# Kernel tuning notes

Hardware: AMD Instinct MI355X
Metric: run time of the kernel (lower is better)

The kernel has to match this reference:

```python
import jax, jax.numpy as jnp
import numpy as np

NUM_PARTS = 24  # SMPL body parts


def setup_inputs() -> dict:
    key = jax.random.key(0)
    k1, k2, k3 = jax.random.split(key, 3)
    B, N, C = 64, 16384, 128
    xyz = jax.random.normal(k1, (B, N, 3), dtype=jnp.float32)
    features = jax.random.normal(k2, (B, C, N), dtype=jnp.float32)
    labels = jax.random.randint(k3, (B, N), 0, NUM_PARTS, dtype=jnp.int32)
    return {"xyz": xyz, "features": features, "labels": labels}


def reference(xyz, features, labels):
    # xyz: [B,N,3], features: [B,C,N], labels: [B,N] int in [0,24)
    B, N, _ = xyz.shape
    C = features.shape[1]
    K = NUM_PARTS

    onehot = (labels[:, :, None] == jnp.arange(K)[None, None, :]).astype(xyz.dtype)  # [B,N,K]
    counts = onehot.sum(axis=1)                       # [B,K]
    denom = jnp.maximum(counts, 1.0)[:, :, None]      # torch.where(count!=0, count, 1)

    feats_t = jnp.transpose(features, (0, 2, 1))      # [B,N,C]
    mean_xyz = jnp.einsum('bnk,bnc->bkc', onehot, xyz) / denom      # [B,K,3]
    mean_feat = jnp.einsum('bnk,bnc->bkc', onehot, feats_t) / denom  # [B,K,C]
    # (empty segments already yield 0 since the sum is 0; matches non_zero_mask logic)

    # surface branch: per point, subtract its own segment's mean, mask outside
    # segment to 0, then max over all points (zeros included in the original max)
    mean_per_point = jnp.take_along_axis(mean_feat, labels[:, :, None].astype(jnp.int32), axis=1)  # [B,N,C]
    diff = feats_t - mean_per_point                   # [B,N,C]
    seg_ids = (jnp.arange(B, dtype=jnp.int32)[:, None] * K + labels).reshape(-1)  # [B*N]
    seg_max = jax.ops.segment_max(diff.reshape(B * N, C), seg_ids, num_segments=B * K)
    surface = jnp.maximum(seg_max.reshape(B, K, C), 0.0)  # zeros from masked points dominate; empty seg -> 0

    part_features = jnp.concatenate([mean_feat, surface], axis=-1)   # [B,K,2C]
    concat = jnp.concatenate([mean_xyz, part_features], axis=-1)     # [B,K,3+2C] = concatenate_features
    return concat
```

## Files before the change

kernel.cpp:

```cpp
#include <hip/hip_runtime.h>

#define BB 64
#define NN 16384
#define CC 128
#define KK 24
#define OUTW (3 + 2*CC)
#define NCHUNK 16

__global__ __launch_bounds__(256) void k1_cnt_xyz(
    const float* __restrict__ xyz, const int* __restrict__ labels,
    float* __restrict__ pcnt, float* __restrict__ psxyz)
{
    __shared__ float bins[4][KK][4];
    const int tid   = threadIdx.x;
    const int b     = blockIdx.x >> 4;
    const int chunk = blockIdx.x & 15;
    const int w     = tid >> 6;

    for (int i = tid; i < 4*KK*4; i += 256) ((float*)bins)[i] = 0.f;
    __syncthreads();

    const int4*   lrow = (const int4*)(labels + (size_t)b*NN);
    const float4* xrow = (const float4*)(xyz + (size_t)b*NN*3);

    int n4 = chunk*256 + tid;
    int4 l = lrow[n4];
    float4 f0 = xrow[n4*3+0], f1 = xrow[n4*3+1], f2 = xrow[n4*3+2];
    float px[4] = {f0.x, f0.w, f1.z, f2.y};
    float py[4] = {f0.y, f1.x, f1.w, f2.z};
    float pz[4] = {f0.z, f1.y, f2.x, f2.w};
    int   ls[4] = {l.x, l.y, l.z, l.w};
    #pragma unroll
    for (int j = 0; j < 4; ++j) {
        float* bb = bins[w][ls[j]];
        atomicAdd(&bb[0], 1.0f);
        atomicAdd(&bb[1], px[j]);
        atomicAdd(&bb[2], py[j]);
        atomicAdd(&bb[3], pz[j]);
    }
    __syncthreads();
    if (tid < KK*4) {
        int k = tid >> 2, j = tid & 3;
        float v = bins[0][k][j] + bins[1][k][j] + bins[2][k][j] + bins[3][k][j];
        int base = (b*NCHUNK + chunk)*KK + k;
        if (j == 0) pcnt[base] = v;
        else        psxyz[base*3 + (j-1)] = v;
    }
}

__global__ __launch_bounds__(256) void k2_feat(
    const float* __restrict__ features, const int* __restrict__ labels,
    float* __restrict__ sumf, float* __restrict__ maxf)
{
    const int tid  = threadIdx.x;
    const int lane = tid & 63;
    const int wid  = blockIdx.x*4 + (tid >> 6);
    const int b    = wid >> 6;
    const int cp   = wid & 63;

    const float4* f0 = (const float4*)(features + ((size_t)b*CC + cp)*NN);
    const float4* f1 = f0 + (size_t)64*NN/4;
    const int4*   lr = (const int4*)(labels + (size_t)b*NN);

    float s0[KK], s1[KK], m0[KK], m1[KK];
    #pragma unroll
    for (int k = 0; k < KK; ++k) { s0[k]=0.f; s1[k]=0.f; m0[k]=0.f; m1[k]=0.f; }

    for (int it = 0; it < NN/256; ++it) {
        int idx = it*64 + lane;
        float4 a = f0[idx];
        float4 c = f1[idx];
        int4   l = lr[idx];
        #pragma unroll
        for (int k = 0; k < KK; ++k) {
            bool e0 = (l.x == k), e1 = (l.y == k), e2 = (l.z == k), e3 = (l.w == k);
            float t0 = e0 ? a.x : 0.f, t1 = e1 ? a.y : 0.f;
            float t2 = e2 ? a.z : 0.f, t3 = e3 ? a.w : 0.f;
            s0[k] += (t0 + t1) + (t2 + t3);
            m0[k] = fmaxf(fmaxf(m0[k], t0), t1);
            m0[k] = fmaxf(fmaxf(m0[k], t2), t3);
            float u0 = e0 ? c.x : 0.f, u1 = e1 ? c.y : 0.f;
            float u2 = e2 ? c.z : 0.f, u3 = e3 ? c.w : 0.f;
            s1[k] += (u0 + u1) + (u2 + u3);
            m1[k] = fmaxf(fmaxf(m1[k], u0), u1);
            m1[k] = fmaxf(fmaxf(m1[k], u2), u3);
        }
    }

    #pragma unroll
    for (int k = 0; k < KK; ++k) {
        #pragma unroll
        for (int off = 32; off; off >>= 1) {
            s0[k] += __shfl_xor(s0[k], off, 64);
            s1[k] += __shfl_xor(s1[k], off, 64);
            m0[k] = fmaxf(m0[k], __shfl_xor(m0[k], off, 64));
            m1[k] = fmaxf(m1[k], __shfl_xor(m1[k], off, 64));
        }
    }

    if (lane == 0) {
        float* sp = sumf + (size_t)b*KK*CC + cp;
        float* mp = maxf + (size_t)b*KK*CC + cp;
        #pragma unroll
        for (int k = 0; k < KK; ++k) {
            sp[k*CC]      = s0[k];
            sp[k*CC + 64] = s1[k];
            mp[k*CC]      = m0[k];
            mp[k*CC + 64] = m1[k];
        }
    }
}

__global__ __launch_bounds__(128) void k3_final(
    const float* __restrict__ pcnt, const float* __restrict__ psxyz,
    const float* __restrict__ sumf, const float* __restrict__ maxf,
    float* __restrict__ out)
{
    const int bk = blockIdx.x;
    const int b  = bk / KK, k = bk % KK;
    const int c  = threadIdx.x;

    float cn = 0.f;
    #pragma unroll
    for (int ch = 0; ch < NCHUNK; ++ch) cn += pcnt[(b*NCHUNK + ch)*KK + k];
    float inv = 1.0f / fmaxf(cn, 1.0f);

    float* orow = out + (size_t)bk * OUTW;
    if (c < 3) {
        float s = 0.f;
        #pragma unroll
        for (int ch = 0; ch < NCHUNK; ++ch) s += psxyz[((b*NCHUNK + ch)*KK + k)*3 + c];
        orow[c] = s * inv;
    }
    float s    = sumf[(size_t)bk*CC + c];
    float mean = s * inv;
    orow[3 + c] = mean;
    float m    = maxf[(size_t)bk*CC + c];
    orow[3 + CC + c] = (cn > 0.f) ? fmaxf(m - mean, 0.f) : 0.f;
}

extern "C" void kernel_launch(void* const* d_in, const int* in_sizes, int n_in,
                              void* d_out, int out_size, void* d_ws, size_t ws_size,
                              hipStream_t stream) {
    const float* xyz      = (const float*)d_in[0];
    const float* features = (const float*)d_in[1];
    const int*   labels   = (const int*)d_in[2];
    float* out = (float*)d_out;

    char* ws = (char*)d_ws;
    const size_t SZ_SUMF = (size_t)BB*KK*CC*4;
    const size_t SZ_PCNT = (size_t)BB*NCHUNK*KK*4;
    float* sumf  = (float*)ws;
    float* maxf  = (float*)(ws + SZ_SUMF);
    float* pcnt  = (float*)(ws + 2*SZ_SUMF);
    float* psxyz = (float*)(ws + 2*SZ_SUMF + SZ_PCNT);

    k1_cnt_xyz<<<BB*NCHUNK, 256, 0, stream>>>(xyz, labels, pcnt, psxyz);
    k2_feat<<<BB*CC/2/4, 256, 0, stream>>>(features, labels, sumf, maxf);
    k3_final<<<BB*KK, 128, 0, stream>>>(pcnt, psxyz, sumf, maxf, out);
}
```

Measured before the change: 962.2 us.

## Replace per-segment register scan with LDS atomic binning in feature reduction

The feature kernel no longer loops over all 24 segments per element with compare-and-select into register accumulators. Each element is now scattered into shared-memory bins keyed by its label using atomicAdd for sums and integer atomicMax for clamped maxima, with 4 replica slots per wave to spread contention. This removes the 24x redundant ALU work and the large register footprint. In exchange it adds heavy LDS atomic traffic with bank conflicts and serialization when lanes share a label. Float atomic summation order also becomes nondeterministic.

```diff
diff --git a/kernel.cpp b/kernel.cpp
--- a/kernel.cpp
+++ b/kernel.cpp
@@ -52,62 +52,61 @@
     const float* __restrict__ features, const int* __restrict__ labels,
     float* __restrict__ sumf, float* __restrict__ maxf)
 {
+    __shared__ float s_sum[4][KK][4][2];
+    __shared__ int   s_max[4][KK][4][2];
+
     const int tid  = threadIdx.x;
     const int lane = tid & 63;
-    const int wid  = blockIdx.x*4 + (tid >> 6);
+    const int w    = tid >> 6;
+    const int wid  = blockIdx.x*4 + w;
     const int b    = wid >> 6;
     const int cp   = wid & 63;
+    const int r2   = (lane & 3) * 2;
+
+    for (int i = tid; i < 4*KK*4*2; i += 256) {
+        ((float*)s_sum)[i] = 0.f;
+        ((int*)  s_max)[i] = 0;
+    }
+    __syncthreads();
 
     const float4* f0 = (const float4*)(features + ((size_t)b*CC + cp)*NN);
     const float4* f1 = f0 + (size_t)64*NN/4;
     const int4*   lr = (const int4*)(labels + (size_t)b*NN);
 
-    float s0[KK], s1[KK], m0[KK], m1[KK];
-    #pragma unroll
-    for (int k = 0; k < KK; ++k) { s0[k]=0.f; s1[k]=0.f; m0[k]=0.f; m1[k]=0.f; }
+    float* ws_sum = &s_sum[w][0][0][0];
+    int*   ws_max = &s_max[w][0][0][0];
 
     for (int it = 0; it < NN/256; ++it) {
         int idx = it*64 + lane;
         float4 a = f0[idx];
         float4 c = f1[idx];
         int4   l = lr[idx];
+        int   la[4] = {l.x, l.y, l.z, l.w};
+        float va[4] = {a.x, a.y, a.z, a.w};
+        float vc[4] = {c.x, c.y, c.z, c.w};
         #pragma unroll
-        for (int k = 0; k < KK; ++k) {
-            bool e0 = (l.x == k), e1 = (l.y == k), e2 = (l.z == k), e3 = (l.w == k);
-            float t0 = e0 ? a.x : 0.f, t1 = e1 ? a.y : 0.f;
-            float t2 = e2 ? a.z : 0.f, t3 = e3 ? a.w : 0.f;
-            s0[k] += (t0 + t1) + (t2 + t3);
-            m0[k] = fmaxf(fmaxf(m0[k], t0), t1);
-            m0[k] = fmaxf(fmaxf(m0[k], t2), t3);
-            float u0 = e0 ? c.x : 0.f, u1 = e1 ? c.y : 0.f;
-            float u2 = e2 ? c.z : 0.f, u3 = e3 ? c.w : 0.f;
-            s1[k] += (u0 + u1) + (u2 + u3);
-            m1[k] = fmaxf(fmaxf(m1[k], u0), u1);
-            m1[k] = fmaxf(fmaxf(m1[k], u2), u3);
+        for (int j = 0; j < 4; ++j) {
+            int base = la[j]*8 + r2;
+            atomicAdd(&ws_sum[base+0], va[j]);
+            atomicAdd(&ws_sum[base+1], vc[j]);
+            atomicMax(&ws_max[base+0], __float_as_int(fmaxf(va[j], 0.f)));
+            atomicMax(&ws_max[base+1], __float_as_int(fmaxf(vc[j], 0.f)));
         }
     }
+    __syncthreads();
 
-    #pragma unroll
-    for (int k = 0; k < KK; ++k) {
+    if (lane < 48) {
+        int k  = lane >> 1;
+        int ch = lane & 1;
+        float s = 0.f, m = 0.f;
         #pragma unroll
-        for (int off = 32; off; off >>= 1) {
-            s0[k] += __shfl_xor(s0[k], off, 64);
-            s1[k] += __shfl_xor(s1[k], off, 64);
-            m0[k] = fmaxf(m0[k], __shfl_xor(m0[k], off, 64));
-            m1[k] = fmaxf(m1[k], __shfl_xor(m1[k], off, 64));
+        for (int rr = 0; rr < 4; ++rr) {
+            s += s_sum[w][k][rr][ch];
+            m  = fmaxf(m, __int_as_float(s_max[w][k][rr][ch]));
         }
-    }
-
-    if (lane == 0) {
-        float* sp = sumf + (size_t)b*KK*CC + cp;
-        float* mp = maxf + (size_t)b*KK*CC + cp;
-        #pragma unroll
-        for (int k = 0; k < KK; ++k) {
-            sp[k*CC]      = s0[k];
-            sp[k*CC + 64] = s1[k];
-            mp[k*CC]      = m0[k];
-            mp[k*CC + 64] = m1[k];
-        }
+        size_t o = (size_t)b*KK*CC + (size_t)k*CC + cp + (ch ? 64 : 0);
+        sumf[o] = s;
+        maxf[o] = m;
     }
 }
 
```

Result: slower. 1.270 ms (+32.0%).
